# Performance work log

Hardware: AMD Instinct MI355X
Metric: run time of the kernel (lower is better)

The kernel has to match this reference:

```python
import jax, jax.numpy as jnp
import numpy as np

N_NODES = 10000
N_EDGES = 320000
D_NODE = 128
D_EDGE = 32
D_IN = 2 * D_NODE + D_EDGE  # 288, concat(sender, receiver, edge)
D_HID = 192                 # AutoMLP log-spaced hidden dim between 288 and 128
D_OUT = 128


def setup_inputs() -> dict:
    key = jax.random.key(0)
    ks = jax.random.split(key, 8)
    n_embed = jax.random.normal(ks[0], (N_NODES, D_NODE), dtype=jnp.float32)
    e_embed = jax.random.normal(ks[1], (N_EDGES, D_EDGE), dtype=jnp.float32)
    senders = jnp.sort(jax.random.randint(ks[2], (N_EDGES,), 0, N_NODES, dtype=jnp.int32))
    receivers = jax.random.randint(ks[3], (N_EDGES,), 0, N_NODES, dtype=jnp.int32)
    # AutoMLP parameters (lecun_normal-style scaling)
    W1 = jax.random.normal(ks[4], (D_IN, D_HID), dtype=jnp.float32) / np.sqrt(D_IN)
    b1 = jnp.zeros((D_HID,), dtype=jnp.float32)
    W2 = jax.random.normal(ks[5], (D_HID, D_OUT), dtype=jnp.float32) / np.sqrt(D_HID)
    b2 = jnp.zeros((D_OUT,), dtype=jnp.float32)
    return {"n_embed": n_embed, "e_embed": e_embed, "senders": senders,
            "receivers": receivers, "W1": W1, "b1": b1, "W2": W2, "b2": b2}


def reference(n_embed, e_embed, senders, receivers, W1, b1, W2, b2):
    # gather sender/receiver node embeddings and concat with edge features: [E, 288]
    inp = jnp.concatenate([n_embed[senders], n_embed[receivers], e_embed], axis=-1)
    # AutoMLP: Dense -> tanh -> Dense (final layer linear)
    h = jnp.tanh(inp @ W1 + b1)          # [E, 192]
    msg = h @ W2 + b2                    # [E, 128]
    # segment_mean over senders (sorted), num_segments = n_nodes
    seg_sum = jax.ops.segment_sum(msg, senders, num_segments=N_NODES,
                                  indices_are_sorted=True)
    counts = jax.ops.segment_sum(jnp.ones((msg.shape[0],), dtype=msg.dtype), senders,
                                 num_segments=N_NODES, indices_are_sorted=True)
    return seg_sum / jnp.maximum(counts, 1.0)[:, None]
```

## Files before the change

### kernel.cpp

```cpp
#include <hip/hip_runtime.h>

#define E_TOT 320000
#define NN    10000
#define DN    128
#define DE    32
#define DH    192
#define DO    128
#define EB    64
#define SHS   196
#define SMT   68

typedef __attribute__((ext_vector_type(8))) short bf16x8;
typedef __attribute__((ext_vector_type(4))) float f32x4;

#define W1_FRAGS (8*12*64)
#define E_FRAGS  (12*64)
#define W2_FRAGS (6*8*64)
#define FRAGS_TOT (W1_FRAGS + E_FRAGS + W2_FRAGS)
__device__ __align__(16) unsigned short g_p1[W1_FRAGS * 8];
__device__ __align__(16) unsigned short g_e [E_FRAGS * 8];
__device__ __align__(16) unsigned short g_p2[W2_FRAGS * 8];

__device__ __forceinline__ unsigned short f2bf(float f) {
    union { float f; unsigned u; } v; v.f = f;
    return (unsigned short)((v.u + 0x7FFFu + ((v.u >> 16) & 1u)) >> 16);
}
__device__ __forceinline__ float bflo(unsigned u) {
    union { unsigned v; float f; } t; t.v = u << 16; return t.f;
}
__device__ __forceinline__ float bfhi(unsigned u) {
    union { unsigned v; float f; } t; t.v = u & 0xFFFF0000u; return t.f;
}
__device__ __forceinline__ float bf2f(unsigned short s) {
    union { unsigned v; float f; } t; t.v = (unsigned)s << 16; return t.f;
}
__device__ __forceinline__ float tanh_fast(float x) {
    float ex = __expf(x + x);
    return 1.0f - 2.0f * __builtin_amdgcn_rcpf(ex + 1.0f);
}
__device__ __forceinline__ unsigned cvt_pk_bf16(float lo, float hi) {
    unsigned r;
    asm("v_cvt_pk_bf16_f32 %0, %1, %2" : "=v"(r) : "v"(lo), "v"(hi));
    return r;
}

__global__ void prep(const float* __restrict__ W1, const float* __restrict__ W2,
                     const int* __restrict__ senders,
                     float* __restrict__ outz, float* __restrict__ invc)
{
    int f = blockIdx.x * 256 + threadIdx.x;
    unsigned short tmp[8];
    if (f < W1_FRAGS) {
        int kk = f / (12 * 64), nt = (f >> 6) % 12, lane = f & 63;
        int r0 = kk * 32 + ((lane >> 4) << 3);
        int c  = nt * 16 + (lane & 15);
        #pragma unroll
        for (int i = 0; i < 8; ++i) tmp[i] = f2bf(W1[(r0 + i) * DH + c]);
        *(uint4*)(g_p1 + (size_t)f * 8) = *(const uint4*)tmp;
    } else if (f < W1_FRAGS + E_FRAGS) {
        int f2 = f - W1_FRAGS;
        int mt = f2 >> 6, lane = f2 & 63;
        int k0 = ((lane >> 4) << 3);
        int hid = mt * 16 + (lane & 15);
        #pragma unroll
        for (int i = 0; i < 8; ++i) tmp[i] = f2bf(W1[(256 + k0 + i) * DH + hid]);
        *(uint4*)(g_e + (size_t)f2 * 8) = *(const uint4*)tmp;
    } else if (f < FRAGS_TOT) {
        int f3 = f - W1_FRAGS - E_FRAGS;
        int kk = f3 / (8 * 64), nt = (f3 >> 6) % 8, lane = f3 & 63;
        int r0 = kk * 32 + ((lane >> 4) << 3);
        int c  = nt * 16 + (lane & 15);
        #pragma unroll
        for (int i = 0; i < 8; ++i) tmp[i] = f2bf(W2[(r0 + i) * DO + c]);
        *(uint4*)(g_p2 + (size_t)f3 * 8) = *(const uint4*)tmp;
    } else if (f < FRAGS_TOT + NN * DO) {
        outz[f - FRAGS_TOT] = 0.f;
    } else if (f < FRAGS_TOT + NN * DO + NN) {
        int n = f - FRAGS_TOT - NN * DO;
        int lo = 0, hi = E_TOT;
        while (lo < hi) { int m = (lo + hi) >> 1; if (senders[m] < n) lo = m + 1; else hi = m; }
        int s0 = lo;
        hi = E_TOT;
        while (lo < hi) { int m = (lo + hi) >> 1; if (senders[m] < n + 1) lo = m + 1; else hi = m; }
        int cnt = lo - s0;
        invc[n] = (cnt > 1) ? 1.0f / (float)cnt : 1.0f;
    }
}

__global__ __launch_bounds__(256) void node_proj(
    const float* __restrict__ n_embed, const float* __restrict__ b1,
    unsigned short* __restrict__ P)
{
    __shared__ __align__(16) unsigned short s_a[64][136];
    const int tid  = threadIdx.x;
    const int half = blockIdx.y;
    const int n0   = blockIdx.x * 64;

    #pragma unroll
    for (int it = 0; it < 8; ++it) {
        int idx = tid + it * 256;
        int row = idx >> 5, c = idx & 31;
        float4 v = make_float4(0.f, 0.f, 0.f, 0.f);
        if (n0 + row < NN) v = ((const float4*)(n_embed + (size_t)(n0 + row) * DN))[c];
        unsigned t0 = cvt_pk_bf16(v.x, v.y), t1 = cvt_pk_bf16(v.z, v.w);
        *(uint2*)&s_a[row][c * 4] = make_uint2(t0, t1);
    }
    __syncthreads();

    const int lane = tid & 63, w = tid >> 6;
    const int arow = lane & 15, akb = (lane >> 4) * 8, rbase = (lane >> 4) * 4;

    f32x4 acc[4][3];
    #pragma unroll
    for (int mt = 0; mt < 4; ++mt)
        #pragma unroll
        for (int j = 0; j < 3; ++j) acc[mt][j] = (f32x4){0.f, 0.f, 0.f, 0.f};

    for (int kk = 0; kk < 4; ++kk) {
        bf16x8 a[4], b[3];
        #pragma unroll
        for (int mt = 0; mt < 4; ++mt)
            a[mt] = *(const bf16x8*)&s_a[mt * 16 + arow][kk * 32 + akb];
        #pragma unroll
        for (int j = 0; j < 3; ++j)
            b[j] = *(const bf16x8*)(g_p1 + (((size_t)(kk + 4 * half) * 12 + (3 * w + j)) * 64 + lane) * 8);
        #pragma unroll
        for (int mt = 0; mt < 4; ++mt)
            #pragma unroll
            for (int j = 0; j < 3; ++j)
                acc[mt][j] = __builtin_amdgcn_mfma_f32_16x16x32_bf16(a[mt], b[j], acc[mt][j], 0, 0, 0);
    }

    unsigned short* Pout = P + (size_t)half * NN * DH;
    float bj[3];
    #pragma unroll
    for (int j = 0; j < 3; ++j) bj[j] = (half == 0) ? b1[48 * w + 16 * j + arow] : 0.f;
    const int gq = arow >> 2, ii = arow & 3;
    #pragma unroll
    for (int mt = 0; mt < 4; ++mt)
        #pragma unroll
        for (int j = 0; j < 3; ++j)
            #pragma unroll
            for (int r = 0; r < 4; ++r) {
                int row = n0 + mt * 16 + rbase + r;
                if (row < NN)
                    Pout[((size_t)row * 4 + gq) * 48 + (3 * w + j) * 4 + ii] =
                        f2bf(acc[mt][j][r] + bj[j]);
            }
}

__global__ __launch_bounds__(256, 4) void edge_mlp9(
    const float* __restrict__ e_embed,
    const int* __restrict__ senders, const int* __restrict__ receivers,
    const unsigned short* __restrict__ Ps, const unsigned short* __restrict__ Pr,
    const float* __restrict__ b2, const float* __restrict__ invc,
    float* __restrict__ out)
{
    __shared__ __align__(16) char s_u[64 * SHS * 2];
    __shared__ int s_send[EB];
    unsigned short (*s_h)[SHS]    = (unsigned short(*)[SHS])s_u;
    unsigned short (*s_msgT)[SMT] = (unsigned short(*)[SMT])s_u;

    const int tid  = threadIdx.x;
    const int nb8  = gridDim.x >> 3;
    const int e0   = (((blockIdx.x & 7) * nb8) + (blockIdx.x >> 3)) * EB;
    const int lane = tid & 63, w = tid >> 6;
    const int arow = lane & 15, g = lane >> 4;

    const int myedge = e0 + w * 16 + arow;
    const int sN = senders[myedge], rN = receivers[myedge];
    const unsigned short* psbase = Ps + ((size_t)sN * 4 + g) * 48;
    const unsigned short* prbase = Pr + ((size_t)rN * 4 + g) * 48;
    uint4 psq[6], prq[6];
    #pragma unroll
    for (int j = 0; j < 6; ++j) {
        psq[j] = *(const uint4*)(psbase + j * 8);
        prq[j] = *(const uint4*)(prbase + j * 8);
    }
    union { bf16x8 v; unsigned u[4]; } bfr;
    {
        const float* erow = e_embed + (size_t)myedge * DE + g * 8;
        float4 ev0 = *(const float4*)erow;
        float4 ev1 = *(const float4*)(erow + 4);
        bfr.u[0] = cvt_pk_bf16(ev0.x, ev0.y);
        bfr.u[1] = cvt_pk_bf16(ev0.z, ev0.w);
        bfr.u[2] = cvt_pk_bf16(ev1.x, ev1.y);
        bfr.u[3] = cvt_pk_bf16(ev1.z, ev1.w);
    }
    if (tid < EB) s_send[tid] = senders[e0 + tid];

    #pragma unroll
    for (int mt = 0; mt < 12; ++mt) {
        unsigned px, py, qx, qy;
        if ((mt & 1) == 0) {
            px = psq[mt >> 1].x; py = psq[mt >> 1].y;
            qx = prq[mt >> 1].x; qy = prq[mt >> 1].y;
        } else {
            px = psq[mt >> 1].z; py = psq[mt >> 1].w;
            qx = prq[mt >> 1].z; qy = prq[mt >> 1].w;
        }
        bf16x8 af = *(const bf16x8*)(g_e + ((size_t)mt * 64 + lane) * 8);
        f32x4 z = (f32x4){0.f, 0.f, 0.f, 0.f};
        f32x4 acc = __builtin_amdgcn_mfma_f32_16x16x32_bf16(af, bfr.v, z, 0, 0, 0);
        float t0 = tanh_fast(acc[0] + bflo(px) + bflo(qx));
        float t1 = tanh_fast(acc[1] + bfhi(px) + bfhi(qx));
        float t2 = tanh_fast(acc[2] + bflo(py) + bflo(qy));
        float t3 = tanh_fast(acc[3] + bfhi(py) + bfhi(qy));
        *(uint2*)&s_h[w * 16 + arow][mt * 16 + g * 4] =
            make_uint2(cvt_pk_bf16(t0, t1), cvt_pk_bf16(t2, t3));
    }
    __syncthreads();

    f32x4 acc2[4][2];
    #pragma unroll
    for (int mt = 0; mt < 4; ++mt)
        #pragma unroll
        for (int j = 0; j < 2; ++j) acc2[mt][j] = (f32x4){0.f, 0.f, 0.f, 0.f};

    #pragma unroll
    for (int kk = 0; kk < 6; ++kk) {
        union { bf16x8 v; uint2 p[2]; } a[4];
        bf16x8 b[2];
        #pragma unroll
        for (int mt = 0; mt < 4; ++mt) {
            const unsigned short* hp = &s_h[mt * 16 + arow][kk * 32 + g * 8];
            a[mt].p[0] = *(const uint2*)hp;
            a[mt].p[1] = *(const uint2*)(hp + 4);
        }
        #pragma unroll
        for (int j = 0; j < 2; ++j)
            b[j] = *(const bf16x8*)(g_p2 + (((size_t)kk * 8 + (2 * w + j)) * 64 + lane) * 8);
        #pragma unroll
        for (int mt = 0; mt < 4; ++mt)
            #pragma unroll
            for (int j = 0; j < 2; ++j)
                acc2[mt][j] = __builtin_amdgcn_mfma_f32_16x16x32_bf16(a[mt].v, b[j], acc2[mt][j], 0, 0, 0);
    }
    __syncthreads();

    {
        const float bd0 = b2[32 * w + arow], bd1 = b2[32 * w + 16 + arow];
        #pragma unroll
        for (int mt = 0; mt < 4; ++mt) {
            float v0 = acc2[mt][0][0] + bd0, v1 = acc2[mt][0][1] + bd0;
            float v2 = acc2[mt][0][2] + bd0, v3 = acc2[mt][0][3] + bd0;
            *(uint2*)&s_msgT[32 * w + arow][mt * 16 + g * 4] =
                make_uint2(cvt_pk_bf16(v0, v1), cvt_pk_bf16(v2, v3));
            float u0 = acc2[mt][1][0] + bd1, u1 = acc2[mt][1][1] + bd1;
            float u2 = acc2[mt][1][2] + bd1, u3 = acc2[mt][1][3] + bd1;
            *(uint2*)&s_msgT[32 * w + 16 + arow][mt * 16 + g * 4] =
                make_uint2(cvt_pk_bf16(u0, u1), cvt_pk_bf16(u2, u3));
        }
    }
    __syncthreads();

    {
        const int c  = tid & 127;
        const int r0 = (tid >> 7) * 32;
        float vals[32];
        #pragma unroll
        for (int e = 0; e < 32; ++e) vals[e] = bf2f(s_msgT[c][r0 + e]);
        float sum = 0.f;
        int cur = s_send[r0];
        #pragma unroll
        for (int e = 0; e < 32; ++e) {
            sum += vals[e];
            int nxt = (e + 1 < 32) ? s_send[r0 + e + 1] : -1;
            if (nxt != cur) {
                atomicAdd(&out[(size_t)cur * DO + c], sum * invc[cur]);
                sum = 0.f;
                cur = nxt;
            }
        }
    }
}

extern "C" void kernel_launch(void* const* d_in, const int* in_sizes, int n_in,
                              void* d_out, int out_size, void* d_ws, size_t ws_size,
                              hipStream_t stream)
{
    const float* n_embed   = (const float*)d_in[0];
    const float* e_embed   = (const float*)d_in[1];
    const int*   senders   = (const int*)d_in[2];
    const int*   receivers = (const int*)d_in[3];
    const float* W1        = (const float*)d_in[4];
    const float* b1        = (const float*)d_in[5];
    const float* W2        = (const float*)d_in[6];
    const float* b2        = (const float*)d_in[7];
    float* out = (float*)d_out;

    unsigned short* Ps = (unsigned short*)d_ws;
    unsigned short* Pr = Ps + (size_t)NN * DH;
    float*          invc = (float*)(Pr + (size_t)NN * DH);

    const int prep_items = FRAGS_TOT + NN * DO + NN;
    prep<<<(prep_items + 255) / 256, 256, 0, stream>>>(W1, W2, senders, out, invc);
    node_proj<<<dim3((NN + 63) / 64, 2), 256, 0, stream>>>(n_embed, b1, Ps);
    edge_mlp9<<<E_TOT / EB, 256, 0, stream>>>(
        e_embed, senders, receivers, Ps, Pr, b2, invc, out);
}
```

Measured before the change: 85.32 us.

## Halve edge block to 32 edges with 128 threads and move output zeroing to memset

The edge MLP kernel now processes 32 edges per block with 2 waves instead of 64 edges with 4 waves. Each wave covers 64 output columns across 2 M-tiles, and the segment reduction has one thread per column over 32 edges, with packed shared-memory reads. Output zeroing moves from the prep kernel to hipMemsetAsync, which shrinks prep. The aim is less shared memory per block and more blocks for occupancy and tail balance, at the cost of more blocks, more W2 fragment loads per edge, and possibly more atomics at block boundaries.

Result: slower. 94.31 us (+10.5%).

```diff
diff --git a/kernel.cpp b/kernel.cpp
--- a/kernel.cpp
+++ b/kernel.cpp
@@ -6,9 +6,9 @@
 #define DE    32
 #define DH    192
 #define DO    128
-#define EB    64
+#define EB    32
 #define SHS   196
-#define SMT   68
+#define SMT   36
 
 typedef __attribute__((ext_vector_type(8))) short bf16x8;
 typedef __attribute__((ext_vector_type(4))) float f32x4;
@@ -45,8 +45,7 @@
 }
 
 __global__ void prep(const float* __restrict__ W1, const float* __restrict__ W2,
-                     const int* __restrict__ senders,
-                     float* __restrict__ outz, float* __restrict__ invc)
+                     const int* __restrict__ senders, float* __restrict__ invc)
 {
     int f = blockIdx.x * 256 + threadIdx.x;
     unsigned short tmp[8];
@@ -73,10 +72,8 @@
         #pragma unroll
         for (int i = 0; i < 8; ++i) tmp[i] = f2bf(W2[(r0 + i) * DO + c]);
         *(uint4*)(g_p2 + (size_t)f3 * 8) = *(const uint4*)tmp;
-    } else if (f < FRAGS_TOT + NN * DO) {
-        outz[f - FRAGS_TOT] = 0.f;
-    } else if (f < FRAGS_TOT + NN * DO + NN) {
-        int n = f - FRAGS_TOT - NN * DO;
+    } else if (f < FRAGS_TOT + NN) {
+        int n = f - FRAGS_TOT;
         int lo = 0, hi = E_TOT;
         while (lo < hi) { int m = (lo + hi) >> 1; if (senders[m] < n) lo = m + 1; else hi = m; }
         int s0 = lo;
@@ -149,14 +146,14 @@
             }
 }
 
-__global__ __launch_bounds__(256, 4) void edge_mlp9(
+__global__ __launch_bounds__(128) void edge_mlp11(
     const float* __restrict__ e_embed,
     const int* __restrict__ senders, const int* __restrict__ receivers,
     const unsigned short* __restrict__ Ps, const unsigned short* __restrict__ Pr,
     const float* __restrict__ b2, const float* __restrict__ invc,
     float* __restrict__ out)
 {
-    __shared__ __align__(16) char s_u[64 * SHS * 2];
+    __shared__ __align__(16) char s_u[EB * SHS * 2];
     __shared__ int s_send[EB];
     unsigned short (*s_h)[SHS]    = (unsigned short(*)[SHS])s_u;
     unsigned short (*s_msgT)[SMT] = (unsigned short(*)[SMT])s_u;
@@ -211,61 +208,61 @@
     }
     __syncthreads();
 
-    f32x4 acc2[4][2];
-    #pragma unroll
-    for (int mt = 0; mt < 4; ++mt)
-        #pragma unroll
-        for (int j = 0; j < 2; ++j) acc2[mt][j] = (f32x4){0.f, 0.f, 0.f, 0.f};
+    f32x4 acc2[2][4];
+    #pragma unroll
+    for (int mt = 0; mt < 2; ++mt)
+        #pragma unroll
+        for (int j = 0; j < 4; ++j) acc2[mt][j] = (f32x4){0.f, 0.f, 0.f, 0.f};
 
     #pragma unroll
     for (int kk = 0; kk < 6; ++kk) {
-        union { bf16x8 v; uint2 p[2]; } a[4];
-        bf16x8 b[2];
-        #pragma unroll
-        for (int mt = 0; mt < 4; ++mt) {
+        union { bf16x8 v; uint2 p[2]; } a[2];
+        bf16x8 b[4];
+        #pragma unroll
+        for (int mt = 0; mt < 2; ++mt) {
             const unsigned short* hp = &s_h[mt * 16 + arow][kk * 32 + g * 8];
             a[mt].p[0] = *(const uint2*)hp;
             a[mt].p[1] = *(const uint2*)(hp + 4);
         }
         #pragma unroll
-        for (int j = 0; j < 2; ++j)
-            b[j] = *(const bf16x8*)(g_p2 + (((size_t)kk * 8 + (2 * w + j)) * 64 + lane) * 8);
-        #pragma unroll
-        for (int mt = 0; mt < 4; ++mt)
+        for (int j = 0; j < 4; ++j)
+            b[j] = *(const bf16x8*)(g_p2 + (((size_t)kk * 8 + (4 * w + j)) * 64 + lane) * 8);
+        #pragma unroll
+        for (int mt = 0; mt < 2; ++mt)
             #pragma unroll
-            for (int j = 0; j < 2; ++j)
+            for (int j = 0; j < 4; ++j)
                 acc2[mt][j] = __builtin_amdgcn_mfma_f32_16x16x32_bf16(a[mt].v, b[j], acc2[mt][j], 0, 0, 0);
     }
     __syncthreads();
 
+    #pragma unroll
+    for (int j = 0; j < 4; ++j) {
+        const float bd = b2[64 * w + 16 * j + arow];
+        #pragma unroll
+        for (int mt = 0; mt < 2; ++mt) {
+            float v0 = acc2[mt][j][0] + bd, v1 = acc2[mt][j][1] + bd;
+            float v2 = acc2[mt][j][2] + bd, v3 = acc2[mt][j][3] + bd;
+            *(uint2*)&s_msgT[64 * w + 16 * j + arow][mt * 16 + g * 4] =
+                make_uint2(cvt_pk_bf16(v0, v1), cvt_pk_bf16(v2, v3));
+        }
+    }
+    __syncthreads();
+
     {
-        const float bd0 = b2[32 * w + arow], bd1 = b2[32 * w + 16 + arow];
-        #pragma unroll
-        for (int mt = 0; mt < 4; ++mt) {
-            float v0 = acc2[mt][0][0] + bd0, v1 = acc2[mt][0][1] + bd0;
-            float v2 = acc2[mt][0][2] + bd0, v3 = acc2[mt][0][3] + bd0;
-            *(uint2*)&s_msgT[32 * w + arow][mt * 16 + g * 4] =
-                make_uint2(cvt_pk_bf16(v0, v1), cvt_pk_bf16(v2, v3));
-            float u0 = acc2[mt][1][0] + bd1, u1 = acc2[mt][1][1] + bd1;
-            float u2 = acc2[mt][1][2] + bd1, u3 = acc2[mt][1][3] + bd1;
-            *(uint2*)&s_msgT[32 * w + 16 + arow][mt * 16 + g * 4] =
-                make_uint2(cvt_pk_bf16(u0, u1), cvt_pk_bf16(u2, u3));
-        }
-    }
-    __syncthreads();
-
-    {
-        const int c  = tid & 127;
-        const int r0 = (tid >> 7) * 32;
+        const int c = tid;
         float vals[32];
         #pragma unroll
-        for (int e = 0; e < 32; ++e) vals[e] = bf2f(s_msgT[c][r0 + e]);
+        for (int k = 0; k < 8; ++k) {
+            uint2 v = *(const uint2*)&s_msgT[c][k * 4];
+            vals[k * 4 + 0] = bflo(v.x); vals[k * 4 + 1] = bfhi(v.x);
+            vals[k * 4 + 2] = bflo(v.y); vals[k * 4 + 3] = bfhi(v.y);
+        }
         float sum = 0.f;
-        int cur = s_send[r0];
+        int cur = s_send[0];
         #pragma unroll
         for (int e = 0; e < 32; ++e) {
             sum += vals[e];
-            int nxt = (e + 1 < 32) ? s_send[r0 + e + 1] : -1;
+            int nxt = (e + 1 < 32) ? s_send[e + 1] : -1;
             if (nxt != cur) {
                 atomicAdd(&out[(size_t)cur * DO + c], sum * invc[cur]);
                 sum = 0.f;
@@ -293,9 +290,10 @@
     unsigned short* Pr = Ps + (size_t)NN * DH;
     float*          invc = (float*)(Pr + (size_t)NN * DH);
 
-    const int prep_items = FRAGS_TOT + NN * DO + NN;
-    prep<<<(prep_items + 255) / 256, 256, 0, stream>>>(W1, W2, senders, out, invc);
+    hipMemsetAsync(out, 0, (size_t)NN * DO * sizeof(float), stream);
+    const int prep_items = FRAGS_TOT + NN;
+    prep<<<(prep_items + 255) / 256, 256, 0, stream>>>(W1, W2, senders, invc);
     node_proj<<<dim3((NN + 63) / 64, 2), 256, 0, stream>>>(n_embed, b1, Ps);
-    edge_mlp9<<<E_TOT / EB, 256, 0, stream>>>(
+    edge_mlp11<<<E_TOT / EB, 128, 0, stream>>>(
         e_embed, senders, receivers, Ps, Pr, b2, invc, out);
 }
```
